# Performance work log

Hardware: AMD Instinct MI355X
Metric: run time of the kernel (lower is better)

Reference implementation:

```python
import jax, jax.numpy as jnp
import numpy as np

PATCH = 768
POS = 64
HID = 512
B, N = 8, 2048


def setup_inputs() -> dict:
    key = jax.random.key(0)
    ks = jax.random.split(key, 8)
    d_in = PATCH + POS
    s = 1.0 / np.sqrt(d_in)
    return {
        "patches": jax.random.normal(ks[0], (B, N, PATCH), jnp.float32),
        "positions": jax.random.normal(ks[1], (B, N, POS), jnp.float32),
        "Wq": jax.random.uniform(ks[2], (d_in, HID), jnp.float32, -s, s),
        "bq": jax.random.uniform(ks[3], (HID,), jnp.float32, -s, s),
        "Wk": jax.random.uniform(ks[4], (d_in, HID), jnp.float32, -s, s),
        "bk": jax.random.uniform(ks[5], (d_in and HID,), jnp.float32, -s, s),
        "Wv": jax.random.uniform(ks[6], (d_in, HID), jnp.float32, -s, s),
        "bv": jax.random.uniform(ks[7], (HID,), jnp.float32, -s, s),
    }


def reference(patches, positions, Wq, bq, Wk, bk, Wv, bv):
    # concat patch features with positional features: [B, N, PATCH+POS]
    x = jnp.concatenate([patches, positions], axis=-1)
    Q = x @ Wq + bq  # [B, N, HID]
    K = x @ Wk + bk
    V = x @ Wv + bv
    scale = jnp.sqrt(jnp.asarray(HID, x.dtype))
    scores = jnp.einsum("bnd,bmd->bnm", Q, K) / scale  # [B, N, N]
    weights = jax.nn.softmax(scores, axis=-1)
    return jnp.einsum("bnm,bmd->bnd", weights, V)  # [B, N, HID]
```

## Files before the change

kernel.cpp:

```cpp
#include <hip/hip_runtime.h>
#include <hip/hip_bf16.h>
#include <math.h>

typedef __hip_bfloat16 bf16;
typedef __attribute__((ext_vector_type(4))) float f32x4;
typedef __attribute__((ext_vector_type(8))) short s16x8;

typedef const __attribute__((address_space(1))) void gvoid_t;
typedef __attribute__((address_space(3))) void lvoid_t;

__device__ __forceinline__ void gload16(const void* g, void* l) {
  __builtin_amdgcn_global_load_lds((gvoid_t*)g, (lvoid_t*)l, 16, 0, 0);
}
__device__ __forceinline__ unsigned short f2b(float f) {
  bf16 h = __float2bfloat16(f);
  return *(unsigned short*)&h;
}

__global__ __launch_bounds__(256) void prep_x(const float* __restrict__ patches,
                                              const float* __restrict__ positions,
                                              bf16* __restrict__ xb) {
  const long long row = blockIdx.x;
  const int c = threadIdx.x;
  const bool lo = (c < 192);
  const bool hi = (c >= 192) && (c < 208);
  const float* src = lo ? (patches + row * 768 + c * 4)
                        : (positions + row * 64 + (c - 192) * 4);
  if (lo || hi) {
    float4 v = *(const float4*)src;
    const int dst = lo ? (c * 4) : (768 + (c - 192) * 4);
    uint2 w;
    w.x = (unsigned int)f2b(v.x) | ((unsigned int)f2b(v.y) << 16);
    w.y = (unsigned int)f2b(v.z) | ((unsigned int)f2b(v.w) << 16);
    *(uint2*)(xb + row * 832 + dst) = w;
  }
}

__global__ __launch_bounds__(256) void prep_w(const float* __restrict__ Wq,
                                              const float* __restrict__ Wk,
                                              const float* __restrict__ Wv,
                                              bf16* __restrict__ Wt) {
  __shared__ float tile[32][33];
  const int z = blockIdx.z;
  const float* W = (z == 0) ? Wq : (z == 1) ? Wk : Wv;
  bf16* T = Wt + (long long)z * 512 * 832;
  const int n0 = blockIdx.x * 32;
  const int k0 = blockIdx.y * 32;
  const int tx = threadIdx.x, ty = threadIdx.y;
  #pragma unroll
  for (int i = 0; i < 32; i += 8)
    tile[ty + i][tx] = W[(long long)(k0 + ty + i) * 512 + n0 + tx];
  __syncthreads();
  #pragma unroll
  for (int i = 0; i < 32; i += 8)
    T[(long long)(n0 + ty + i) * 832 + k0 + tx] = __float2bfloat16(tile[tx][ty + i]);
}

__global__ __launch_bounds__(256) void gemm_qkv(
    const bf16* __restrict__ xb, const bf16* __restrict__ Wt,
    const float* __restrict__ bq, const float* __restrict__ bk,
    const float* __restrict__ bv,
    bf16* __restrict__ qk, bf16* __restrict__ vt) {
  __shared__ bf16 As[128 * 64];
  __shared__ bf16 Bs[128 * 64];
  const int tid = threadIdx.x;
  const int wave = tid >> 6, lane = tid & 63;
  const int llo = lane & 15, lhi = lane >> 4;
  const int wm = wave >> 1, wn = wave & 1;

  const unsigned int lin = blockIdx.x;
  const unsigned int xcd = lin & 7u, idx = lin >> 3;
  const unsigned int g = xcd * 192u + idx;
  const unsigned int bm_t = g / 12u;
  const unsigned int bn_t = g - bm_t * 12u;
  const int row0 = (int)bm_t * 128;
  const int col0 = (int)bn_t * 128;
  const int z = col0 >> 9;

  f32x4 acc[4][4] = {};

  for (int kt = 0; kt < 832; kt += 64) {
    #pragma unroll
    for (int i = 0; i < 4; i++) {
      const int c = i * 256 + tid;
      const int r = c >> 3, cc = c & 7;
      const int kk = (cc ^ (r & 7)) << 3;
      gload16(xb + ((long long)(row0 + r) * 832 + kt + kk),
              (char*)As + (long long)(i * 256 + wave * 64) * 16);
      gload16(Wt + ((long long)(col0 + r) * 832 + kt + kk),
              (char*)Bs + (long long)(i * 256 + wave * 64) * 16);
    }
    __syncthreads();
    #pragma unroll
    for (int k0 = 0; k0 < 64; k0 += 32) {
      const int xk = ((((k0 >> 3) + lhi) ^ (llo & 7)) << 3);
      s16x8 af[4], bfr[4];
      #pragma unroll
      for (int mf = 0; mf < 4; mf++)
        af[mf] = *(const s16x8*)&As[(wm * 64 + mf * 16 + llo) * 64 + xk];
      #pragma unroll
      for (int nf = 0; nf < 4; nf++)
        bfr[nf] = *(const s16x8*)&Bs[(wn * 64 + nf * 16 + llo) * 64 + xk];
      #pragma unroll
      for (int mf = 0; mf < 4; mf++)
        #pragma unroll
        for (int nf = 0; nf < 4; nf++)
          acc[mf][nf] = __builtin_amdgcn_mfma_f32_16x16x32_bf16(
              af[mf], bfr[nf], acc[mf][nf], 0, 0, 0);
    }
    __syncthreads();
  }

  if (z < 2) {
    const float* bias = z ? bk : bq;
    bf16* outp = qk + (long long)z * 16384 * 512;
    #pragma unroll
    for (int mf = 0; mf < 4; mf++)
      #pragma unroll
      for (int nf = 0; nf < 4; nf++) {
        const int c = (col0 & 511) + wn * 64 + nf * 16 + llo;
        const int grow0 = row0 + wm * 64 + mf * 16 + lhi * 4;
        const float bb = bias[c];
        #pragma unroll
        for (int r = 0; r < 4; r++)
          outp[(long long)(grow0 + r) * 512 + c] =
              __float2bfloat16(acc[mf][nf][r] + bb);
      }
  } else {
    #pragma unroll
    for (int mf = 0; mf < 4; mf++)
      #pragma unroll
      for (int nf = 0; nf < 4; nf++) {
        const int c = (col0 & 511) + wn * 64 + nf * 16 + llo;
        const int grow0 = row0 + wm * 64 + mf * 16 + lhi * 4;
        const int b = grow0 >> 11, j = grow0 & 2047;
        const float bb = bv[c];
        uint2 w;
        w.x = (unsigned int)f2b(acc[mf][nf][0] + bb) |
              ((unsigned int)f2b(acc[mf][nf][1] + bb) << 16);
        w.y = (unsigned int)f2b(acc[mf][nf][2] + bb) |
              ((unsigned int)f2b(acc[mf][nf][3] + bb) << 16);
        *(uint2*)(vt + (long long)b * 512 * 2048 + (long long)c * 2048 + j) = w;
      }
  }
}

#define VMW8 asm volatile("s_waitcnt vmcnt(8)" ::: "memory")
#define PBAR do { __builtin_amdgcn_s_barrier(); __builtin_amdgcn_sched_barrier(0); } while (0)

__device__ __forceinline__ void stage_half(const bf16* src, char* lds) {
  gload16(src, lds);
  gload16(src + 64 * 512, lds + 8192);
}
__device__ __forceinline__ void lda4(const bf16* base, int rowbase, int llo,
                                     int xk0, int xk1, s16x8 af[4][2]) {
  #pragma unroll
  for (int mf = 0; mf < 4; mf++) {
    const bf16* p = base + (rowbase + mf * 16 + llo) * 64;
    af[mf][0] = *(const s16x8*)(p + xk0);
    af[mf][1] = *(const s16x8*)(p + xk1);
  }
}
__device__ __forceinline__ void ldb2(const bf16* base, int rowbase, int llo,
                                     int xk0, int xk1, s16x8 bfr[2][2]) {
  #pragma unroll
  for (int nf = 0; nf < 2; nf++) {
    const bf16* p = base + (rowbase + nf * 16 + llo) * 64;
    bfr[nf][0] = *(const s16x8*)(p + xk0);
    bfr[nf][1] = *(const s16x8*)(p + xk1);
  }
}
__device__ __forceinline__ void mma16(f32x4 acc[4][2], s16x8 af[4][2],
                                      s16x8 bfr[2][2]) {
  __builtin_amdgcn_s_setprio(1);
  #pragma unroll
  for (int mf = 0; mf < 4; mf++)
    #pragma unroll
    for (int nf = 0; nf < 2; nf++) {
      acc[mf][nf] = __builtin_amdgcn_mfma_f32_16x16x32_bf16(
          af[mf][0], bfr[nf][0], acc[mf][nf], 0, 0, 0);
      acc[mf][nf] = __builtin_amdgcn_mfma_f32_16x16x32_bf16(
          af[mf][1], bfr[nf][1], acc[mf][nf], 0, 0, 0);
    }
  __builtin_amdgcn_s_setprio(0);
}

__global__ __launch_bounds__(512, 2) void gemm_scores(const bf16* __restrict__ qk,
                                                      bf16* __restrict__ S,
                                                      float* __restrict__ rowsumP) {
  __shared__ bf16 As[2][256 * 64];
  __shared__ bf16 Bs[2][256 * 64];
  const int tid = threadIdx.x;
  const int wave = tid >> 6, lane = tid & 63;
  const int llo = lane & 15, lhi = lane >> 4;
  const int wm = wave >> 2, wn = wave & 3;

  const unsigned int lin = blockIdx.x;
  const int b = (int)(lin & 7u);
  const unsigned int idx = lin >> 3;
  const int row0 = (int)(idx >> 3) * 256;
  const int coltile = (int)(idx & 7u);
  const int col0 = coltile * 256;

  const bf16* Ab = qk + (long long)b * 2048 * 512;
  const bf16* Bb = qk + (long long)16384 * 512 + (long long)b * 2048 * 512;

  const int sr = tid >> 3;
  const int kkofs = ((tid & 7) ^ (sr & 7)) << 3;
  const bf16* sA = Ab + (long long)(row0 + sr) * 512 + kkofs;
  const bf16* sB = Bb + (long long)(col0 + sr) * 512 + kkofs;
  const int wofs = wave * 1024;

  const int xk0 = ((lhi ^ (llo & 7)) << 3);
  const int xk1 = (((4 + lhi) ^ (llo & 7)) << 3);

  f32x4 acc[2][2][4][2] = {};
  s16x8 af[4][2], bf0[2][2], bf1[2][2];

  stage_half(sA, (char*)As[0] + wofs);
  stage_half(sB, (char*)Bs[0] + wofs);
  stage_half(sB + 128 * 512, (char*)Bs[0] + 16384 + wofs);
  stage_half(sA + 128 * 512, (char*)As[0] + 16384 + wofs);
  stage_half(sA + 64, (char*)As[1] + wofs);
  stage_half(sB + 64, (char*)Bs[1] + wofs);
  VMW8;
  PBAR;

  for (int i = 0; i < 4; ++i) {
    const int kt1 = (2 * i + 1) * 64;
    const int kt2 = (2 * i + 2 < 8) ? (2 * i + 2) * 64 : 448;
    const int kt3 = (2 * i + 3 < 8) ? (2 * i + 3) * 64 : 448;
    lda4(As[0], wm * 64, llo, xk0, xk1, af);
    ldb2(Bs[0], wn * 32, llo, xk0, xk1, bf0);
    stage_half(sB + 128 * 512 + kt1, (char*)Bs[1] + 16384 + wofs);
    VMW8; PBAR;
    mma16(acc[0][0], af, bf0);
    ldb2(Bs[0], 128 + wn * 32, llo, xk0, xk1, bf1);
    stage_half(sA + 128 * 512 + kt1, (char*)As[1] + 16384 + wofs);
    VMW8; PBAR;
    mma16(acc[0][1], af, bf1);
    lda4(As[0], 128 + wm * 64, llo, xk0, xk1, af);
    stage_half(sA + kt2, (char*)As[0] + wofs);
    PBAR;
    mma16(acc[1][0], af, bf0);
    stage_half(sB + kt2, (char*)Bs[0] + wofs);
    VMW8; PBAR;
    mma16(acc[1][1], af, bf1);
    lda4(As[1], wm * 64, llo, xk0, xk1, af);
    ldb2(Bs[1], wn * 32, llo, xk0, xk1, bf0);
    stage_half(sB + 128 * 512 + kt2, (char*)Bs[0] + 16384 + wofs);
    VMW8; PBAR;
    mma16(acc[0][0], af, bf0);
    ldb2(Bs[1], 128 + wn * 32, llo, xk0, xk1, bf1);
    stage_half(sA + 128 * 512 + kt2, (char*)As[0] + 16384 + wofs);
    VMW8; PBAR;
    mma16(acc[0][1], af, bf1);
    lda4(As[1], 128 + wm * 64, llo, xk0, xk1, af);
    stage_half(sA + kt3, (char*)As[1] + wofs);
    PBAR;
    mma16(acc[1][0], af, bf0);
    stage_half(sB + kt3, (char*)Bs[1] + wofs);
    VMW8; PBAR;
    mma16(acc[1][1], af, bf1);
  }

  __syncthreads();

  const float alpha = 0.044194173824159216f;
  bf16* Sb = S + (long long)b * 2048 * 2048;
  #pragma unroll
  for (int qr = 0; qr < 2; qr++)
    #pragma unroll
    for (int qc = 0; qc < 2; qc++)
      #pragma unroll
      for (int mf = 0; mf < 4; mf++)
        #pragma unroll
        for (int nf = 0; nf < 2; nf++) {
          #pragma unroll
          for (int r = 0; r < 4; r++)
            acc[qr][qc][mf][nf][r] = __expf(acc[qr][qc][mf][nf][r] * alpha);
          const int gcol = col0 + qc * 128 + wn * 32 + nf * 16 + llo;
          const int grow0 = row0 + qr * 128 + wm * 64 + mf * 16 + lhi * 4;
          #pragma unroll
          for (int r = 0; r < 4; r++)
            Sb[(long long)(grow0 + r) * 2048 + gcol] =
                __float2bfloat16(acc[qr][qc][mf][nf][r]);
        }

  float* psum = (float*)As;
  #pragma unroll
  for (int qr = 0; qr < 2; qr++)
    #pragma unroll
    for (int mf = 0; mf < 4; mf++)
      #pragma unroll
      for (int r = 0; r < 4; r++) {
        float p = acc[qr][0][mf][0][r] + acc[qr][0][mf][1][r] +
                  acc[qr][1][mf][0][r] + acc[qr][1][mf][1][r];
        p += __shfl_xor(p, 1, 64);
        p += __shfl_xor(p, 2, 64);
        p += __shfl_xor(p, 4, 64);
        p += __shfl_xor(p, 8, 64);
        if (llo == 0)
          psum[wn * 256 + qr * 128 + wm * 64 + mf * 16 + lhi * 4 + r] = p;
      }
  __syncthreads();
  if (tid < 256) {
    const float v = psum[tid] + psum[256 + tid] + psum[512 + tid] + psum[768 + tid];
    rowsumP[(long long)(b * 8 + coltile) * 2048 + row0 + tid] = v;
  }
}

__global__ __launch_bounds__(256) void reduce_rowsum(
    const float* __restrict__ rowsumP, float* __restrict__ rinv) {
  const int i = blockIdx.x * 256 + threadIdx.x;
  const int b = i >> 11, row = i & 2047;
  const float* p = rowsumP + ((long long)b * 8) * 2048 + row;
  float s = 0.f;
  #pragma unroll
  for (int t = 0; t < 8; t++) s += p[t * 2048];
  rinv[i] = 1.0f / s;
}

__global__ __launch_bounds__(256) void gemm_pv(const bf16* __restrict__ S,
                                               const bf16* __restrict__ vt,
                                               const float* __restrict__ rinv,
                                               float* __restrict__ out) {
  __shared__ bf16 As[128 * 64];
  __shared__ bf16 Bs[128 * 64];
  const int tid = threadIdx.x;
  const int wave = tid >> 6, lane = tid & 63;
  const int llo = lane & 15, lhi = lane >> 4;
  const int wm = wave >> 1, wn = wave & 1;

  const unsigned int lin = blockIdx.x;
  const unsigned int xcd = lin & 7u, idx = lin >> 3;
  const int b = (int)xcd;
  const int row0 = (int)(idx >> 2) * 128;
  const int col0 = (int)(idx & 3u) * 128;

  const bf16* Ab = S + (long long)b * 2048 * 2048;
  const bf16* Bb = vt + (long long)b * 512 * 2048;

  f32x4 acc[4][4] = {};
  for (int kt = 0; kt < 2048; kt += 64) {
    #pragma unroll
    for (int i = 0; i < 4; i++) {
      const int c = i * 256 + tid;
      const int r = c >> 3, cc = c & 7;
      const int kk = (cc ^ (r & 7)) << 3;
      gload16(Ab + ((long long)(row0 + r) * 2048 + kt + kk),
              (char*)As + (long long)(i * 256 + wave * 64) * 16);
      gload16(Bb + ((long long)(col0 + r) * 2048 + kt + kk),
              (char*)Bs + (long long)(i * 256 + wave * 64) * 16);
    }
    __syncthreads();
    #pragma unroll
    for (int k0 = 0; k0 < 64; k0 += 32) {
      const int xk = ((((k0 >> 3) + lhi) ^ (llo & 7)) << 3);
      s16x8 af[4], bfr[4];
      #pragma unroll
      for (int mf = 0; mf < 4; mf++)
        af[mf] = *(const s16x8*)&As[(wm * 64 + mf * 16 + llo) * 64 + xk];
      #pragma unroll
      for (int nf = 0; nf < 4; nf++)
        bfr[nf] = *(const s16x8*)&Bs[(wn * 64 + nf * 16 + llo) * 64 + xk];
      #pragma unroll
      for (int mf = 0; mf < 4; mf++)
        #pragma unroll
        for (int nf = 0; nf < 4; nf++)
          acc[mf][nf] = __builtin_amdgcn_mfma_f32_16x16x32_bf16(
              af[mf], bfr[nf], acc[mf][nf], 0, 0, 0);
    }
    __syncthreads();
  }

  const float* rs = rinv + (long long)b * 2048;
  float* Ob = out + (long long)b * 2048 * 512;
  #pragma unroll
  for (int mf = 0; mf < 4; mf++) {
    const int grow0 = row0 + wm * 64 + mf * 16 + lhi * 4;
    float iv[4];
    #pragma unroll
    for (int r = 0; r < 4; r++) iv[r] = rs[grow0 + r];
    #pragma unroll
    for (int nf = 0; nf < 4; nf++) {
      const int gcol = col0 + wn * 64 + nf * 16 + llo;
      #pragma unroll
      for (int r = 0; r < 4; r++)
        Ob[(long long)(grow0 + r) * 512 + gcol] = acc[mf][nf][r] * iv[r];
    }
  }
}

extern "C" void kernel_launch(void* const* d_in, const int* in_sizes, int n_in,
                              void* d_out, int out_size, void* d_ws, size_t ws_size,
                              hipStream_t stream) {
  const float* patches = (const float*)d_in[0];
  const float* positions = (const float*)d_in[1];
  const float* Wq = (const float*)d_in[2];
  const float* bq = (const float*)d_in[3];
  const float* Wk = (const float*)d_in[4];
  const float* bk = (const float*)d_in[5];
  const float* Wv = (const float*)d_in[6];
  const float* bv = (const float*)d_in[7];
  float* out = (float*)d_out;

  if (ws_size < 149422080u) return;

  char* ws = (char*)d_ws;
  bf16* Wt = (bf16*)(ws);
  bf16* xb = (bf16*)(ws + 2555904);
  bf16* qk = (bf16*)(ws + 29818880);
  bf16* vt = (bf16*)(ws + 63373312);
  bf16* S  = (bf16*)(ws + 80150528);
  float* rinv    = (float*)(ws + 147259392);
  float* rowsumP = (float*)(ws + 147324928);

  prep_x<<<16384, 256, 0, stream>>>(patches, positions, xb);
  prep_w<<<dim3(16, 26, 3), dim3(32, 8), 0, stream>>>(Wq, Wk, Wv, Wt);
  gemm_qkv<<<1536, 256, 0, stream>>>(xb, Wt, bq, bk, bv, qk, vt);
  gemm_scores<<<512, 512, 0, stream>>>(qk, S, rowsumP);
  reduce_rowsum<<<64, 256, 0, stream>>>(rowsumP, rinv);
  gemm_pv<<<512, 256, 0, stream>>>(S, vt, rinv, out);
}
```

Before: 272.4 us.

## Rewrite QKV projection GEMM with 256x256 tiles and double-buffered pipelined staging

Measured after the change: 261.6 us. 4.0% less time.

```diff
diff --git a/kernel.cpp b/kernel.cpp
--- a/kernel.cpp
+++ b/kernel.cpp
@@ -56,101 +56,12 @@
     T[(long long)(n0 + ty + i) * 832 + k0 + tx] = __float2bfloat16(tile[tx][ty + i]);
 }
 
-__global__ __launch_bounds__(256) void gemm_qkv(
-    const bf16* __restrict__ xb, const bf16* __restrict__ Wt,
-    const float* __restrict__ bq, const float* __restrict__ bk,
-    const float* __restrict__ bv,
-    bf16* __restrict__ qk, bf16* __restrict__ vt) {
-  __shared__ bf16 As[128 * 64];
-  __shared__ bf16 Bs[128 * 64];
-  const int tid = threadIdx.x;
-  const int wave = tid >> 6, lane = tid & 63;
-  const int llo = lane & 15, lhi = lane >> 4;
-  const int wm = wave >> 1, wn = wave & 1;
-
-  const unsigned int lin = blockIdx.x;
-  const unsigned int xcd = lin & 7u, idx = lin >> 3;
-  const unsigned int g = xcd * 192u + idx;
-  const unsigned int bm_t = g / 12u;
-  const unsigned int bn_t = g - bm_t * 12u;
-  const int row0 = (int)bm_t * 128;
-  const int col0 = (int)bn_t * 128;
-  const int z = col0 >> 9;
-
-  f32x4 acc[4][4] = {};
-
-  for (int kt = 0; kt < 832; kt += 64) {
-    #pragma unroll
-    for (int i = 0; i < 4; i++) {
-      const int c = i * 256 + tid;
-      const int r = c >> 3, cc = c & 7;
-      const int kk = (cc ^ (r & 7)) << 3;
-      gload16(xb + ((long long)(row0 + r) * 832 + kt + kk),
-              (char*)As + (long long)(i * 256 + wave * 64) * 16);
-      gload16(Wt + ((long long)(col0 + r) * 832 + kt + kk),
-              (char*)Bs + (long long)(i * 256 + wave * 64) * 16);
-    }
-    __syncthreads();
-    #pragma unroll
-    for (int k0 = 0; k0 < 64; k0 += 32) {
-      const int xk = ((((k0 >> 3) + lhi) ^ (llo & 7)) << 3);
-      s16x8 af[4], bfr[4];
-      #pragma unroll
-      for (int mf = 0; mf < 4; mf++)
-        af[mf] = *(const s16x8*)&As[(wm * 64 + mf * 16 + llo) * 64 + xk];
-      #pragma unroll
-      for (int nf = 0; nf < 4; nf++)
-        bfr[nf] = *(const s16x8*)&Bs[(wn * 64 + nf * 16 + llo) * 64 + xk];
-      #pragma unroll
-      for (int mf = 0; mf < 4; mf++)
-        #pragma unroll
-        for (int nf = 0; nf < 4; nf++)
-          acc[mf][nf] = __builtin_amdgcn_mfma_f32_16x16x32_bf16(
-              af[mf], bfr[nf], acc[mf][nf], 0, 0, 0);
-    }
-    __syncthreads();
-  }
-
-  if (z < 2) {
-    const float* bias = z ? bk : bq;
-    bf16* outp = qk + (long long)z * 16384 * 512;
-    #pragma unroll
-    for (int mf = 0; mf < 4; mf++)
-      #pragma unroll
-      for (int nf = 0; nf < 4; nf++) {
-        const int c = (col0 & 511) + wn * 64 + nf * 16 + llo;
-        const int grow0 = row0 + wm * 64 + mf * 16 + lhi * 4;
-        const float bb = bias[c];
-        #pragma unroll
-        for (int r = 0; r < 4; r++)
-          outp[(long long)(grow0 + r) * 512 + c] =
-              __float2bfloat16(acc[mf][nf][r] + bb);
-      }
-  } else {
-    #pragma unroll
-    for (int mf = 0; mf < 4; mf++)
-      #pragma unroll
-      for (int nf = 0; nf < 4; nf++) {
-        const int c = (col0 & 511) + wn * 64 + nf * 16 + llo;
-        const int grow0 = row0 + wm * 64 + mf * 16 + lhi * 4;
-        const int b = grow0 >> 11, j = grow0 & 2047;
-        const float bb = bv[c];
-        uint2 w;
-        w.x = (unsigned int)f2b(acc[mf][nf][0] + bb) |
-              ((unsigned int)f2b(acc[mf][nf][1] + bb) << 16);
-        w.y = (unsigned int)f2b(acc[mf][nf][2] + bb) |
-              ((unsigned int)f2b(acc[mf][nf][3] + bb) << 16);
-        *(uint2*)(vt + (long long)b * 512 * 2048 + (long long)c * 2048 + j) = w;
-      }
-  }
-}
-
 #define VMW8 asm volatile("s_waitcnt vmcnt(8)" ::: "memory")
 #define PBAR do { __builtin_amdgcn_s_barrier(); __builtin_amdgcn_sched_barrier(0); } while (0)
 
-__device__ __forceinline__ void stage_half(const bf16* src, char* lds) {
+__device__ __forceinline__ void stage_half(const bf16* src, char* lds, int stride) {
   gload16(src, lds);
-  gload16(src + 64 * 512, lds + 8192);
+  gload16(src + 64 * stride, lds + 8192);
 }
 __device__ __forceinline__ void lda4(const bf16* base, int rowbase, int llo,
                                      int xk0, int xk1, s16x8 af[4][2]) {
@@ -183,6 +94,138 @@
           af[mf][1], bfr[nf][1], acc[mf][nf], 0, 0, 0);
     }
   __builtin_amdgcn_s_setprio(0);
+}
+
+__global__ __launch_bounds__(512, 2) void gemm_qkv(
+    const bf16* __restrict__ xb, const bf16* __restrict__ Wt,
+    const float* __restrict__ bq, const float* __restrict__ bk,
+    const float* __restrict__ bv,
+    bf16* __restrict__ qk, bf16* __restrict__ vt) {
+  __shared__ bf16 As[2][256 * 64];
+  __shared__ bf16 Bs[2][256 * 64];
+  const int tid = threadIdx.x;
+  const int wave = tid >> 6, lane = tid & 63;
+  const int llo = lane & 15, lhi = lane >> 4;
+  const int wm = wave >> 2, wn = wave & 3;
+
+  const unsigned int lin = blockIdx.x;
+  const unsigned int xcd = lin & 7u, idx = lin >> 3;
+  const unsigned int g = xcd * 48u + idx;
+  const unsigned int bm_t = g / 6u;
+  const unsigned int bn_t = g - bm_t * 6u;
+  const int row0 = (int)bm_t * 256;
+  const int col0 = (int)bn_t * 256;
+  const int z = col0 >> 9;
+
+  const int sr = tid >> 3;
+  const int kkofs = ((tid & 7) ^ (sr & 7)) << 3;
+  const bf16* sA = xb + (long long)(row0 + sr) * 832 + kkofs;
+  const bf16* sB = Wt + (long long)(col0 + sr) * 832 + kkofs;
+  const int wofs = wave * 1024;
+
+  const int xk0 = ((lhi ^ (llo & 7)) << 3);
+  const int xk1 = (((4 + lhi) ^ (llo & 7)) << 3);
+
+  f32x4 acc[2][2][4][2] = {};
+  s16x8 af[4][2], bf0[2][2], bf1[2][2];
+
+  stage_half(sA, (char*)As[0] + wofs, 832);
+  stage_half(sB, (char*)Bs[0] + wofs, 832);
+  stage_half(sB + 128 * 832, (char*)Bs[0] + 16384 + wofs, 832);
+  stage_half(sA + 128 * 832, (char*)As[0] + 16384 + wofs, 832);
+  stage_half(sA + 64, (char*)As[1] + wofs, 832);
+  stage_half(sB + 64, (char*)Bs[1] + wofs, 832);
+  VMW8; PBAR;
+
+  for (int i = 0; i < 6; ++i) {
+    const int kt1 = (2 * i + 1) * 64;
+    const int kt2 = (2 * i + 2 <= 12) ? (2 * i + 2) * 64 : 768;
+    const int kt3 = (2 * i + 3 <= 12) ? (2 * i + 3) * 64 : 768;
+    lda4(As[0], wm * 64, llo, xk0, xk1, af);
+    ldb2(Bs[0], wn * 32, llo, xk0, xk1, bf0);
+    stage_half(sB + 128 * 832 + kt1, (char*)Bs[1] + 16384 + wofs, 832);
+    VMW8; PBAR;
+    mma16(acc[0][0], af, bf0);
+    ldb2(Bs[0], 128 + wn * 32, llo, xk0, xk1, bf1);
+    stage_half(sA + 128 * 832 + kt1, (char*)As[1] + 16384 + wofs, 832);
+    VMW8; PBAR;
+    mma16(acc[0][1], af, bf1);
+    lda4(As[0], 128 + wm * 64, llo, xk0, xk1, af);
+    stage_half(sA + kt2, (char*)As[0] + wofs, 832);
+    PBAR;
+    mma16(acc[1][0], af, bf0);
+    stage_half(sB + kt2, (char*)Bs[0] + wofs, 832);
+    VMW8; PBAR;
+    mma16(acc[1][1], af, bf1);
+    lda4(As[1], wm * 64, llo, xk0, xk1, af);
+    ldb2(Bs[1], wn * 32, llo, xk0, xk1, bf0);
+    stage_half(sB + 128 * 832 + kt2, (char*)Bs[0] + 16384 + wofs, 832);
+    VMW8; PBAR;
+    mma16(acc[0][0], af, bf0);
+    ldb2(Bs[1], 128 + wn * 32, llo, xk0, xk1, bf1);
+    stage_half(sA + 128 * 832 + kt2, (char*)As[0] + 16384 + wofs, 832);
+    VMW8; PBAR;
+    mma16(acc[0][1], af, bf1);
+    lda4(As[1], 128 + wm * 64, llo, xk0, xk1, af);
+    stage_half(sA + kt3, (char*)As[1] + wofs, 832);
+    PBAR;
+    mma16(acc[1][0], af, bf0);
+    stage_half(sB + kt3, (char*)Bs[1] + wofs, 832);
+    VMW8; PBAR;
+    mma16(acc[1][1], af, bf1);
+  }
+
+  asm volatile("s_waitcnt vmcnt(4)" ::: "memory");
+  PBAR;
+  lda4(As[0], wm * 64, llo, xk0, xk1, af);
+  ldb2(Bs[0], wn * 32, llo, xk0, xk1, bf0);
+  ldb2(Bs[0], 128 + wn * 32, llo, xk0, xk1, bf1);
+  mma16(acc[0][0], af, bf0);
+  mma16(acc[0][1], af, bf1);
+  lda4(As[0], 128 + wm * 64, llo, xk0, xk1, af);
+  mma16(acc[1][0], af, bf0);
+  mma16(acc[1][1], af, bf1);
+
+  if (z < 2) {
+    const float* bias = z ? bk : bq;
+    bf16* outp = qk + (long long)z * 16384 * 512;
+    #pragma unroll
+    for (int qr = 0; qr < 2; qr++)
+      #pragma unroll
+      for (int qc = 0; qc < 2; qc++)
+        #pragma unroll
+        for (int mf = 0; mf < 4; mf++)
+          #pragma unroll
+          for (int nf = 0; nf < 2; nf++) {
+            const int c = (col0 & 511) + qc * 128 + wn * 32 + nf * 16 + llo;
+            const int grow0 = row0 + qr * 128 + wm * 64 + mf * 16 + lhi * 4;
+            const float bb = bias[c];
+            #pragma unroll
+            for (int r = 0; r < 4; r++)
+              outp[(long long)(grow0 + r) * 512 + c] =
+                  __float2bfloat16(acc[qr][qc][mf][nf][r] + bb);
+          }
+  } else {
+    #pragma unroll
+    for (int qr = 0; qr < 2; qr++)
+      #pragma unroll
+      for (int qc = 0; qc < 2; qc++)
+        #pragma unroll
+        for (int mf = 0; mf < 4; mf++)
+          #pragma unroll
+          for (int nf = 0; nf < 2; nf++) {
+            const int c = (col0 & 511) + qc * 128 + wn * 32 + nf * 16 + llo;
+            const int grow0 = row0 + qr * 128 + wm * 64 + mf * 16 + lhi * 4;
+            const int b = grow0 >> 11, j = grow0 & 2047;
+            const float bb = bv[c];
+            uint2 w;
+            w.x = (unsigned int)f2b(acc[qr][qc][mf][nf][0] + bb) |
+                  ((unsigned int)f2b(acc[qr][qc][mf][nf][1] + bb) << 16);
+            w.y = (unsigned int)f2b(acc[qr][qc][mf][nf][2] + bb) |
+                  ((unsigned int)f2b(acc[qr][qc][mf][nf][3] + bb) << 16);
+            *(uint2*)(vt + (long long)b * 512 * 2048 + (long long)c * 2048 + j) = w;
+          }
+  }
 }
 
 __global__ __launch_bounds__(512, 2) void gemm_scores(const bf16* __restrict__ qk,
@@ -217,14 +260,13 @@
   f32x4 acc[2][2][4][2] = {};
   s16x8 af[4][2], bf0[2][2], bf1[2][2];
 
-  stage_half(sA, (char*)As[0] + wofs);
-  stage_half(sB, (char*)Bs[0] + wofs);
-  stage_half(sB + 128 * 512, (char*)Bs[0] + 16384 + wofs);
-  stage_half(sA + 128 * 512, (char*)As[0] + 16384 + wofs);
-  stage_half(sA + 64, (char*)As[1] + wofs);
-  stage_half(sB + 64, (char*)Bs[1] + wofs);
-  VMW8;
-  PBAR;
+  stage_half(sA, (char*)As[0] + wofs, 512);
+  stage_half(sB, (char*)Bs[0] + wofs, 512);
+  stage_half(sB + 128 * 512, (char*)Bs[0] + 16384 + wofs, 512);
+  stage_half(sA + 128 * 512, (char*)As[0] + 16384 + wofs, 512);
+  stage_half(sA + 64, (char*)As[1] + wofs, 512);
+  stage_half(sB + 64, (char*)Bs[1] + wofs, 512);
+  VMW8; PBAR;
 
   for (int i = 0; i < 4; ++i) {
     const int kt1 = (2 * i + 1) * 64;
@@ -232,34 +274,34 @@
     const int kt3 = (2 * i + 3 < 8) ? (2 * i + 3) * 64 : 448;
     lda4(As[0], wm * 64, llo, xk0, xk1, af);
     ldb2(Bs[0], wn * 32, llo, xk0, xk1, bf0);
-    stage_half(sB + 128 * 512 + kt1, (char*)Bs[1] + 16384 + wofs);
+    stage_half(sB + 128 * 512 + kt1, (char*)Bs[1] + 16384 + wofs, 512);
     VMW8; PBAR;
     mma16(acc[0][0], af, bf0);
     ldb2(Bs[0], 128 + wn * 32, llo, xk0, xk1, bf1);
-    stage_half(sA + 128 * 512 + kt1, (char*)As[1] + 16384 + wofs);
+    stage_half(sA + 128 * 512 + kt1, (char*)As[1] + 16384 + wofs, 512);
     VMW8; PBAR;
     mma16(acc[0][1], af, bf1);
     lda4(As[0], 128 + wm * 64, llo, xk0, xk1, af);
-    stage_half(sA + kt2, (char*)As[0] + wofs);
+    stage_half(sA + kt2, (char*)As[0] + wofs, 512);
     PBAR;
     mma16(acc[1][0], af, bf0);
-    stage_half(sB + kt2, (char*)Bs[0] + wofs);
+    stage_half(sB + kt2, (char*)Bs[0] + wofs, 512);
     VMW8; PBAR;
     mma16(acc[1][1], af, bf1);
     lda4(As[1], wm * 64, llo, xk0, xk1, af);
     ldb2(Bs[1], wn * 32, llo, xk0, xk1, bf0);
-    stage_half(sB + 128 * 512 + kt2, (char*)Bs[0] + 16384 + wofs);
+    stage_half(sB + 128 * 512 + kt2, (char*)Bs[0] + 16384 + wofs, 512);
     VMW8; PBAR;
     mma16(acc[0][0], af, bf0);
     ldb2(Bs[1], 128 + wn * 32, llo, xk0, xk1, bf1);
-    stage_half(sA + 128 * 512 + kt2, (char*)As[0] + 16384 + wofs);
+    stage_half(sA + 128 * 512 + kt2, (char*)As[0] + 16384 + wofs, 512);
     VMW8; PBAR;
     mma16(acc[0][1], af, bf1);
     lda4(As[1], 128 + wm * 64, llo, xk0, xk1, af);
-    stage_half(sA + kt3, (char*)As[1] + wofs);
+    stage_half(sA + kt3, (char*)As[1] + wofs, 512);
     PBAR;
     mma16(acc[1][0], af, bf0);
-    stage_half(sB + kt3, (char*)Bs[1] + wofs);
+    stage_half(sB + kt3, (char*)Bs[1] + wofs, 512);
     VMW8; PBAR;
     mma16(acc[1][1], af, bf1);
   }
@@ -418,7 +460,7 @@
 
   prep_x<<<16384, 256, 0, stream>>>(patches, positions, xb);
   prep_w<<<dim3(16, 26, 3), dim3(32, 8), 0, stream>>>(Wq, Wk, Wv, Wt);
-  gemm_qkv<<<1536, 256, 0, stream>>>(xb, Wt, bq, bk, bv, qk, vt);
+  gemm_qkv<<<384, 512, 0, stream>>>(xb, Wt, bq, bk, bv, qk, vt);
   gemm_scores<<<512, 512, 0, stream>>>(qk, S, rowsumP);
   reduce_rowsum<<<64, 256, 0, stream>>>(rowsumP, rinv);
   gemm_pv<<<512, 256, 0, stream>>>(S, vt, rinv, out);
```
